# Kernel optimization log

Measured on AMD Instinct MI355X. Metric: run time of the kernel, lower is better.

Reference implementation:

```python
import jax, jax.numpy as jnp
import numpy as np

CHUNK = 64  # rows of `a` processed per step to bound the [chunk, N, d] abs-diff intermediate
TAIL_K = 4          # selection_tail_size
FAR_K = 64          # far_sample_count
PUSH_K = 4          # pushing_sample_size
HUBER_DELTA = 1.0   # torch.nn.HuberLoss default


def cdist_l1(a, b):
    # a: [M, d], b: [N, d] -> [M, N] Manhattan distances, computed in row chunks
    M, d = a.shape
    def f(a_chunk):  # [CHUNK, d] -> [CHUNK, N]
        return jnp.abs(a_chunk[:, None, :] - b[None, :, :]).sum(-1)
    return jax.lax.map(f, a.reshape(-1, CHUNK, d)).reshape(M, b.shape[0])


def smallest_k_mean(dists, k):
    # mean of the k smallest entries along last dim
    neg_vals, _ = jax.lax.top_k(-dists, k)
    return (-neg_vals).mean(-1)


def huber(x):
    # HuberLoss(pred=x, target=0), delta=1
    ax = jnp.abs(x)
    return jnp.where(ax < HUBER_DELTA, 0.5 * x * x, HUBER_DELTA * (ax - 0.5 * HUBER_DELTA))


def setup_inputs() -> dict:
    key = jax.random.key(0)
    k1, k2 = jax.random.split(key)
    space_samples = jax.random.normal(k1, (2048, 256), dtype=jnp.float32)
    latents = jax.random.normal(k2, (8192, 256), dtype=jnp.float32)
    return {"space_samples": space_samples, "latents": latents}


def reference(space_samples, latents):
    # space_samples: [M, d] drawn from latent_sampler; latents: [N, d]
    space_dists = cdist_l1(space_samples, latents)            # [M, N]
    tail_dists = smallest_k_mean(space_dists, TAIL_K)          # [M]
    far_inds = jax.lax.top_k(tail_dists, FAR_K)[1]             # [FAR_K]
    far_samples = space_samples[far_inds]                      # [FAR_K, d]
    empty_dists = cdist_l1(far_samples, latents)               # [FAR_K, N]
    close_dists = smallest_k_mean(empty_dists, PUSH_K)         # [FAR_K]
    return huber(close_dists).mean()
```

## Files before the change

kernel.cpp:

```cpp
#include <hip/hip_runtime.h>
#include <hip/hip_bf16.h>


static constexpr int M = 2048;
static constexpr int N = 8192;
static constexpr int KQ = 64;
static constexpr int BKQ = 8;
static constexpr int NSTEP = KQ / BKQ;
static constexpr int ROWS_PER_BLK = 128;
static constexpr int COLS_PER_BLK = 128;
static constexpr int NCHUNK = N / COLS_PER_BLK;
static constexpr int SLD_RED = 68;
static constexpr int BUFU = 2048;

static constexpr float QS  = 21.0f;
static constexpr float QB  = 126.0f;
static constexpr float INV_QS = 1.0f / 21.0f;

__device__ __forceinline__ float med3f(float a, float b, float c) {
    return __builtin_amdgcn_fmed3f(a, b, c);
}

__device__ __forceinline__ void ins4(float d, float& s0, float& s1, float& s2, float& s3) {
    float n0 = fminf(s0, d);
    float n1 = med3f(s0, s1, d);
    float n2 = med3f(s1, s2, d);
    float n3 = med3f(s2, s3, d);
    s0 = n0; s1 = n1; s2 = n2; s3 = n3;
}

__device__ __forceinline__ unsigned int sad8(unsigned int a, unsigned int b, unsigned int c) {
#if __has_builtin(__builtin_amdgcn_sad_u8)
    return __builtin_amdgcn_sad_u8(a, b, c);
#else
    unsigned int d;
    asm("v_sad_u8 %0, %1, %2, %3" : "=v"(d) : "v"(a), "v"(b), "v"(c));
    return d;
#endif
}

__device__ __forceinline__ unsigned int quant4(const float4 v) {
    const float y0 = fminf(fmaxf(fmaf(v.x, QS, QB), 0.0f), 255.0f);
    const float y1 = fminf(fmaxf(fmaf(v.y, QS, QB), 0.0f), 255.0f);
    const float y2 = fminf(fmaxf(fmaf(v.z, QS, QB), 0.0f), 255.0f);
    const float y3 = fminf(fmaxf(fmaf(v.w, QS, QB), 0.0f), 255.0f);
    const unsigned int b0 = (unsigned int)(int)rintf(y0);
    const unsigned int b1 = (unsigned int)(int)rintf(y1);
    const unsigned int b2 = (unsigned int)(int)rintf(y2);
    const unsigned int b3 = (unsigned int)(int)rintf(y3);
    return b0 | (b1 << 8) | (b2 << 16) | (b3 << 24);
}

__device__ __forceinline__ float huber_pos(float x) {
    const float ax = __builtin_fabsf(x);
    return (ax < 1.0f) ? (0.5f * x * x) : (ax - 0.5f);
}

__global__ __launch_bounds__(256)
void convert_kernel(const float* __restrict__ A, const float* __restrict__ B,
                    unsigned int* __restrict__ At, unsigned int* __restrict__ Bt) {
    __shared__ unsigned int lt[KQ * 65];
    const int tid = threadIdx.x;
    const bool isB = (blockIdx.x < N / 64);
    const float* src = isB ? B : A;
    unsigned int* dst = isB ? Bt : At;
    const int rows = isB ? N : M;
    const int r0 = (isB ? blockIdx.x : (blockIdx.x - N / 64)) * 64;

#pragma unroll
    for (int it = 0; it < 16; ++it) {
        const int qi = it * 256 + tid;
        const int row = qi >> 6;
        const int kq = qi & 63;
        const float4 v = *(const float4*)&src[(r0 + row) * 256 + 4 * kq];
        lt[kq * 65 + row] = quant4(v);
    }
    __syncthreads();
#pragma unroll
    for (int it = 0; it < 16; ++it) {
        const int wi = it * 256 + tid;
        const int row = wi & 63;
        const int kq = wi >> 6;
        dst[(size_t)kq * rows + r0 + row] = lt[kq * 65 + row];
    }
}

__global__ __launch_bounds__(256, 4)
void dist4_kernel(const unsigned int* __restrict__ At, const unsigned int* __restrict__ Bt,
                  float4* __restrict__ ws_dist) {
    __shared__ __align__(16) char smem[34816];
    unsigned int* tiles = (unsigned int*)smem;
    const int tid = threadIdx.x;
    const int tx = tid & 15;
    const int ty = tid >> 4;
    const int bx = blockIdx.x;
    const int by = blockIdx.y;
    const int rowBase = by * ROWS_PER_BLK;
    const int colBase = bx * COLS_PER_BLK;

    const int sKq = tid >> 5;
    const int sC  = (tid & 31) * 4;

    unsigned int acc[8][8];
#pragma unroll
    for (int i = 0; i < 8; ++i)
#pragma unroll
        for (int j = 0; j < 8; ++j) acc[i][j] = 0u;

    {
        const uint4 pa = *(const uint4*)&At[sKq * M + rowBase + sC];
        const uint4 pb = *(const uint4*)&Bt[sKq * N + colBase + sC];
        *(uint4*)&tiles[sKq * 128 + sC] = pa;
        *(uint4*)&tiles[1024 + sKq * 128 + sC] = pb;
    }

    int rb = 0;
    int wb = BUFU;
    for (int t0 = 0; t0 < NSTEP; ++t0) {
        __syncthreads();
        uint4 pa, pb;
        const bool pf = (t0 + 1 < NSTEP);
        if (pf) {
            const int kb = (t0 + 1) * BKQ;
            pa = *(const uint4*)&At[(kb + sKq) * M + rowBase + sC];
            pb = *(const uint4*)&Bt[(kb + sKq) * N + colBase + sC];
        }

#pragma unroll
        for (int kq = 0; kq < 4; ++kq) {
            const uint4 aw0 = *(const uint4*)&tiles[rb + kq * 128 + 8 * ty];
            const uint4 aw1 = *(const uint4*)&tiles[rb + kq * 128 + 8 * ty + 4];
            const uint4 bw0 = *(const uint4*)&tiles[rb + 1024 + kq * 128 + 4 * tx];
            const uint4 bw1 = *(const uint4*)&tiles[rb + 1024 + kq * 128 + 64 + 4 * tx];
            const unsigned int a[8] = {aw0.x, aw0.y, aw0.z, aw0.w, aw1.x, aw1.y, aw1.z, aw1.w};
            const unsigned int b[8] = {bw0.x, bw0.y, bw0.z, bw0.w, bw1.x, bw1.y, bw1.z, bw1.w};
#pragma unroll
            for (int i = 0; i < 8; ++i)
#pragma unroll
                for (int j = 0; j < 8; ++j)
                    acc[i][j] = sad8(a[i], b[j], acc[i][j]);
        }

        if (pf) {
            *(uint4*)&tiles[wb + sKq * 128 + sC] = pa;
            *(uint4*)&tiles[wb + 1024 + sKq * 128 + sC] = pb;
        }

#pragma unroll
        for (int kq = 4; kq < 8; ++kq) {
            const uint4 aw0 = *(const uint4*)&tiles[rb + kq * 128 + 8 * ty];
            const uint4 aw1 = *(const uint4*)&tiles[rb + kq * 128 + 8 * ty + 4];
            const uint4 bw0 = *(const uint4*)&tiles[rb + 1024 + kq * 128 + 4 * tx];
            const uint4 bw1 = *(const uint4*)&tiles[rb + 1024 + kq * 128 + 64 + 4 * tx];
            const unsigned int a[8] = {aw0.x, aw0.y, aw0.z, aw0.w, aw1.x, aw1.y, aw1.z, aw1.w};
            const unsigned int b[8] = {bw0.x, bw0.y, bw0.z, bw0.w, bw1.x, bw1.y, bw1.z, bw1.w};
#pragma unroll
            for (int i = 0; i < 8; ++i)
#pragma unroll
                for (int j = 0; j < 8; ++j)
                    acc[i][j] = sad8(a[i], b[j], acc[i][j]);
        }

        rb = (rb == 2 * BUFU) ? 0 : rb + BUFU;
        wb = (wb == 2 * BUFU) ? 0 : wb + BUFU;
    }

    float s[8][4];
#pragma unroll
    for (int i = 0; i < 8; ++i) {
        float s0 = 1e30f, s1 = 1e30f, s2 = 1e30f, s3 = 1e30f;
#pragma unroll
        for (int j = 0; j < 8; ++j) {
            const float d = (float)acc[i][j] * INV_QS;
            ins4(d, s0, s1, s2, s3);
        }
        s[i][0] = s0; s[i][1] = s1; s[i][2] = s2; s[i][3] = s3;
    }

    __syncthreads();
    float (*red)[SLD_RED] = (float (*)[SLD_RED])smem;
#pragma unroll
    for (int i = 0; i < 8; ++i) {
        *(float4*)&red[8 * ty + i][4 * tx] = make_float4(s[i][0], s[i][1], s[i][2], s[i][3]);
    }
    __syncthreads();

    if (tid < ROWS_PER_BLK) {
        float s0 = 1e30f, s1 = 1e30f, s2 = 1e30f, s3 = 1e30f;
#pragma unroll
        for (int c = 0; c < 16; ++c) {
            const float4 v = *(const float4*)&red[tid][4 * c];
            ins4(v.x, s0, s1, s2, s3);
            ins4(v.y, s0, s1, s2, s3);
            ins4(v.z, s0, s1, s2, s3);
            ins4(v.w, s0, s1, s2, s3);
        }
        ws_dist[bx * M + rowBase + tid] = make_float4(s0, s1, s2, s3);
    }
}

__global__ __launch_bounds__(256)
void tail_kernel(const float4* __restrict__ ws_dist, float* __restrict__ tail) {
    const int gtid = blockIdx.x * 256 + threadIdx.x;
    const int row = gtid >> 3;
    const int q = gtid & 7;
    float s0 = 1e30f, s1 = 1e30f, s2 = 1e30f, s3 = 1e30f;
#pragma unroll
    for (int c = 0; c < 8; ++c) {
        const float4 v = ws_dist[(q * 8 + c) * M + row];
        ins4(v.x, s0, s1, s2, s3);
        ins4(v.y, s0, s1, s2, s3);
        ins4(v.z, s0, s1, s2, s3);
        ins4(v.w, s0, s1, s2, s3);
    }
#pragma unroll
    for (int lvl = 1; lvl <= 4; lvl <<= 1) {
        const float o0 = __shfl_xor(s0, lvl, 64);
        const float o1 = __shfl_xor(s1, lvl, 64);
        const float o2 = __shfl_xor(s2, lvl, 64);
        const float o3 = __shfl_xor(s3, lvl, 64);
        ins4(o0, s0, s1, s2, s3);
        ins4(o1, s0, s1, s2, s3);
        ins4(o2, s0, s1, s2, s3);
        ins4(o3, s0, s1, s2, s3);
    }
    if (q == 0) tail[row] = (s0 + s1 + s2 + s3) * 0.25f;
}

__global__ __launch_bounds__(1024)
void top64_kernel(const float* __restrict__ tail, float* __restrict__ out) {
    __shared__ unsigned int hist[8][256];
    __shared__ unsigned int ctrl[2];
    __shared__ float wsum[16];
    __shared__ unsigned int wcnt[16];
    const int tid = threadIdx.x;
    const int wid = tid >> 6;
    const int lane = tid & 63;

    const unsigned int k0 = __float_as_uint(tail[tid]);
    const unsigned int k1 = __float_as_uint(tail[tid + 1024]);

    if (tid == 0) { ctrl[0] = 0u; ctrl[1] = 64u; }

    for (int p = 0; p < 4; ++p) {
        const int shift = 24 - 8 * p;
        ((unsigned int*)hist)[tid] = 0u;
        ((unsigned int*)hist)[tid + 1024] = 0u;
        __syncthreads();
        const unsigned int prefix = ctrl[0];
        const unsigned int t = ctrl[1];
        bool c0 = true, c1 = true;
        if (p > 0) {
            const int sh8 = shift + 8;
            c0 = ((k0 >> sh8) == (prefix >> sh8));
            c1 = ((k1 >> sh8) == (prefix >> sh8));
        }
        if (c0) atomicAdd(&hist[wid & 7][(k0 >> shift) & 255], 1u);
        if (c1) atomicAdd(&hist[wid & 7][(k1 >> shift) & 255], 1u);
        __syncthreads();
        if (tid < 256) {
            unsigned int h = 0;
#pragma unroll
            for (int r = 0; r < 8; ++r) h += hist[r][tid];
            hist[0][tid] = h;
        }
        __syncthreads();
        if (wid == 0) {
            const unsigned int s4 = hist[0][4 * lane] + hist[0][4 * lane + 1] +
                                    hist[0][4 * lane + 2] + hist[0][4 * lane + 3];
            unsigned int suf = s4;
#pragma unroll
            for (int off = 1; off < 64; off <<= 1) {
                const unsigned int v = __shfl_down(suf, off, 64);
                if (lane + off < 64) suf += v;
            }
            const unsigned long long mask = __ballot(suf >= t);
            const int lstar = 63 - __clzll(mask);
            if (lane == lstar) {
                unsigned int c = suf - s4;
                for (int d = 4 * lstar + 3; d >= 4 * lstar; --d) {
                    const unsigned int cd = hist[0][d];
                    c += cd;
                    if (c >= t) {
                        ctrl[0] = prefix | ((unsigned int)d << shift);
                        ctrl[1] = t - (c - cd);
                        break;
                    }
                }
            }
        }
        __syncthreads();
    }

    const unsigned int T = ctrl[0];
    float sum = 0.0f;
    unsigned int cnt = 0;
    if (k0 > T) { ++cnt; sum += huber_pos(__uint_as_float(k0)); }
    if (k1 > T) { ++cnt; sum += huber_pos(__uint_as_float(k1)); }
#pragma unroll
    for (int off = 32; off > 0; off >>= 1) {
        sum += __shfl_down(sum, off, 64);
        cnt += __shfl_down(cnt, off, 64);
    }
    if (lane == 0) { wsum[wid] = sum; wcnt[wid] = cnt; }
    __syncthreads();
    if (tid == 0) {
        float S = 0.0f;
        unsigned int C = 0;
#pragma unroll
        for (int w = 0; w < 16; ++w) { S += wsum[w]; C += wcnt[w]; }
        const float hT = huber_pos(__uint_as_float(T));
        out[0] = (S + (float)(64u - C) * hT) * (1.0f / 64.0f);
    }
}

extern "C" void kernel_launch(void* const* d_in, const int* in_sizes, int n_in,
                              void* d_out, int out_size, void* d_ws, size_t ws_size,
                              hipStream_t stream) {
    const float* A = (const float*)d_in[0];
    const float* B = (const float*)d_in[1];
    float* out = (float*)d_out;

    unsigned int* Bt = (unsigned int*)d_ws;
    unsigned int* At = (unsigned int*)((char*)d_ws + (size_t)KQ * N * 4);
    float4* ws_dist = (float4*)((char*)d_ws + (size_t)KQ * N * 4 + (size_t)KQ * M * 4);
    float* tail = (float*)((char*)ws_dist + (size_t)NCHUNK * M * sizeof(float4));

    convert_kernel<<<dim3(N / 64 + M / 64), 256, 0, stream>>>(A, B, At, Bt);
    dist4_kernel<<<dim3(NCHUNK, M / ROWS_PER_BLK), 256, 0, stream>>>(At, Bt, ws_dist);
    tail_kernel<<<dim3(M * 8 / 256), 256, 0, stream>>>(ws_dist, tail);
    top64_kernel<<<1, 1024, 0, stream>>>(tail, out);
}
```

Measured before the change: 127.3 us.

## Stage SAD tiles via direct global-to-LDS loads with larger K step and LDS prefetch

Replaces the register-staged triple-buffered tile copy with async global_load_lds (16-byte) transfers into a double buffer, and doubles the K step per iteration so there are fewer barriers. The inner loop software-pipelines LDS reads by loading the next quad-slice into registers while v_sad_u8 works on the current one. This is meant to cut VGPR staging, barrier count and LDS-read latency exposure. It risks needing more shared memory (32KB of tiles) and relies on the barrier correctly waiting for the async LDS DMA writes.

```diff
diff --git a/kernel.cpp b/kernel.cpp
--- a/kernel.cpp
+++ b/kernel.cpp
@@ -5,13 +5,12 @@
 static constexpr int M = 2048;
 static constexpr int N = 8192;
 static constexpr int KQ = 64;
-static constexpr int BKQ = 8;
+static constexpr int BKQ = 16;
 static constexpr int NSTEP = KQ / BKQ;
 static constexpr int ROWS_PER_BLK = 128;
 static constexpr int COLS_PER_BLK = 128;
 static constexpr int NCHUNK = N / COLS_PER_BLK;
 static constexpr int SLD_RED = 68;
-static constexpr int BUFU = 2048;
 
 static constexpr float QS  = 21.0f;
 static constexpr float QB  = 126.0f;
@@ -37,6 +36,12 @@
     asm("v_sad_u8 %0, %1, %2, %3" : "=v"(d) : "v"(a), "v"(b), "v"(c));
     return d;
 #endif
+}
+
+__device__ __forceinline__ void gll16(const unsigned int* g, unsigned int* l) {
+    __builtin_amdgcn_global_load_lds(
+        (const __attribute__((address_space(1))) unsigned int*)g,
+        (__attribute__((address_space(3))) unsigned int*)l, 16, 0, 0);
 }
 
 __device__ __forceinline__ unsigned int quant4(const float4 v) {
@@ -107,62 +112,50 @@
 #pragma unroll
         for (int j = 0; j < 8; ++j) acc[i][j] = 0u;
 
-    {
-        const uint4 pa = *(const uint4*)&At[sKq * M + rowBase + sC];
-        const uint4 pb = *(const uint4*)&Bt[sKq * N + colBase + sC];
-        *(uint4*)&tiles[sKq * 128 + sC] = pa;
-        *(uint4*)&tiles[1024 + sKq * 128 + sC] = pb;
-    }
-
-    int rb = 0;
-    int wb = BUFU;
+    auto STAGE = [&](int t, int bufofs) {
+        const int kb = t * BKQ;
+        gll16(&At[(kb + sKq) * M + rowBase + sC],     tiles + bufofs + sKq * 128 + sC);
+        gll16(&At[(kb + sKq + 8) * M + rowBase + sC], tiles + bufofs + (sKq + 8) * 128 + sC);
+        gll16(&Bt[(kb + sKq) * N + colBase + sC],     tiles + bufofs + 2048 + sKq * 128 + sC);
+        gll16(&Bt[(kb + sKq + 8) * N + colBase + sC], tiles + bufofs + 2048 + (sKq + 8) * 128 + sC);
+    };
+
+    auto LDQ = [&](const unsigned int* As, const unsigned int* Bs, int kq,
+                   uint4& a0, uint4& a1, uint4& b0, uint4& b1) {
+        a0 = *(const uint4*)&As[kq * 128 + 8 * ty];
+        a1 = *(const uint4*)&As[kq * 128 + 8 * ty + 4];
+        b0 = *(const uint4*)&Bs[kq * 128 + 4 * tx];
+        b1 = *(const uint4*)&Bs[kq * 128 + 64 + 4 * tx];
+    };
+
+    auto SADQ = [&](const uint4& aw0, const uint4& aw1, const uint4& bw0, const uint4& bw1) {
+        const unsigned int a[8] = {aw0.x, aw0.y, aw0.z, aw0.w, aw1.x, aw1.y, aw1.z, aw1.w};
+        const unsigned int b[8] = {bw0.x, bw0.y, bw0.z, bw0.w, bw1.x, bw1.y, bw1.z, bw1.w};
+#pragma unroll
+        for (int i = 0; i < 8; ++i)
+#pragma unroll
+            for (int j = 0; j < 8; ++j)
+                acc[i][j] = sad8(a[i], b[j], acc[i][j]);
+    };
+
+    STAGE(0, 0);
+
     for (int t0 = 0; t0 < NSTEP; ++t0) {
         __syncthreads();
-        uint4 pa, pb;
-        const bool pf = (t0 + 1 < NSTEP);
-        if (pf) {
-            const int kb = (t0 + 1) * BKQ;
-            pa = *(const uint4*)&At[(kb + sKq) * M + rowBase + sC];
-            pb = *(const uint4*)&Bt[(kb + sKq) * N + colBase + sC];
-        }
-
-#pragma unroll
-        for (int kq = 0; kq < 4; ++kq) {
-            const uint4 aw0 = *(const uint4*)&tiles[rb + kq * 128 + 8 * ty];
-            const uint4 aw1 = *(const uint4*)&tiles[rb + kq * 128 + 8 * ty + 4];
-            const uint4 bw0 = *(const uint4*)&tiles[rb + 1024 + kq * 128 + 4 * tx];
-            const uint4 bw1 = *(const uint4*)&tiles[rb + 1024 + kq * 128 + 64 + 4 * tx];
-            const unsigned int a[8] = {aw0.x, aw0.y, aw0.z, aw0.w, aw1.x, aw1.y, aw1.z, aw1.w};
-            const unsigned int b[8] = {bw0.x, bw0.y, bw0.z, bw0.w, bw1.x, bw1.y, bw1.z, bw1.w};
-#pragma unroll
-            for (int i = 0; i < 8; ++i)
-#pragma unroll
-                for (int j = 0; j < 8; ++j)
-                    acc[i][j] = sad8(a[i], b[j], acc[i][j]);
-        }
-
-        if (pf) {
-            *(uint4*)&tiles[wb + sKq * 128 + sC] = pa;
-            *(uint4*)&tiles[wb + 1024 + sKq * 128 + sC] = pb;
-        }
-
-#pragma unroll
-        for (int kq = 4; kq < 8; ++kq) {
-            const uint4 aw0 = *(const uint4*)&tiles[rb + kq * 128 + 8 * ty];
-            const uint4 aw1 = *(const uint4*)&tiles[rb + kq * 128 + 8 * ty + 4];
-            const uint4 bw0 = *(const uint4*)&tiles[rb + 1024 + kq * 128 + 4 * tx];
-            const uint4 bw1 = *(const uint4*)&tiles[rb + 1024 + kq * 128 + 64 + 4 * tx];
-            const unsigned int a[8] = {aw0.x, aw0.y, aw0.z, aw0.w, aw1.x, aw1.y, aw1.z, aw1.w};
-            const unsigned int b[8] = {bw0.x, bw0.y, bw0.z, bw0.w, bw1.x, bw1.y, bw1.z, bw1.w};
-#pragma unroll
-            for (int i = 0; i < 8; ++i)
-#pragma unroll
-                for (int j = 0; j < 8; ++j)
-                    acc[i][j] = sad8(a[i], b[j], acc[i][j]);
-        }
-
-        rb = (rb == 2 * BUFU) ? 0 : rb + BUFU;
-        wb = (wb == 2 * BUFU) ? 0 : wb + BUFU;
+        if (t0 + 1 < NSTEP) STAGE(t0 + 1, ((t0 + 1) & 1) * 4096);
+
+        const unsigned int* As = tiles + (t0 & 1) * 4096;
+        const unsigned int* Bs = As + 2048;
+
+        uint4 eA0, eA1, eB0, eB1, oA0, oA1, oB0, oB1;
+        LDQ(As, Bs, 0, eA0, eA1, eB0, eB1);
+#pragma unroll
+        for (int h = 0; h < 8; ++h) {
+            LDQ(As, Bs, 2 * h + 1, oA0, oA1, oB0, oB1);
+            SADQ(eA0, eA1, eB0, eB1);
+            if (h < 7) LDQ(As, Bs, 2 * h + 2, eA0, eA1, eB0, eB1);
+            SADQ(oA0, oA1, oB0, oB1);
+        }
     }
 
     float s[8][4];
```

New measurement: 112.0 us. -12.0%, faster.
